# Kernel tuning notes

Measured on AMD Instinct MI355X. Metric: run time of the kernel, lower is better.

Reference implementation:

```python
import jax, jax.numpy as jnp
import numpy as np

N = 50000           # nodes
E = 1_600_000       # edges (avg degree 32)
DIN_N = 128         # in_dim_n
DIN_E = 64          # in_dim_e
DOUT_N = 64         # out_dim_n
DOUT_E = 64         # out_dim_e
SLOPE = 0.01        # torch F.leaky_relu default negative_slope


def _lrelu(x):
    return jnp.where(x >= 0, x, SLOPE * x)


def setup_inputs() -> dict:
    key = jax.random.key(0)
    ks = jax.random.split(key, 8)
    nfeats = jax.random.normal(ks[0], (N, DIN_N), dtype=jnp.float32)
    efeats = jax.random.normal(ks[1], (E, DIN_E), dtype=jnp.float32)
    src = jax.random.randint(ks[2], (E,), 0, N)
    dst = jax.random.randint(ks[3], (E,), 0, N)
    # learned params (xavier-ish scaling)
    W_fc = jax.random.normal(ks[4], (DOUT_N, DIN_N), dtype=jnp.float32) / np.sqrt(DIN_N)
    d_cat = DIN_E + 2 * DOUT_N
    W_edge = jax.random.normal(ks[5], (DOUT_E, d_cat), dtype=jnp.float32) / np.sqrt(d_cat)
    b_edge = jnp.zeros((DOUT_E,), dtype=jnp.float32)
    w_coef = jax.random.normal(ks[6], (1, DOUT_E), dtype=jnp.float32) / np.sqrt(DOUT_E)
    return {"nfeats": nfeats, "efeats": efeats, "src": src, "dst": dst,
            "W_fc": W_fc, "W_edge": W_edge, "b_edge": b_edge, "w_coef": w_coef}


def reference(nfeats, efeats, src, dst, W_fc, W_edge, b_edge, w_coef):
    # node projection: z = fc(nfeats)  (bias=False)
    z = nfeats @ W_fc.T                                   # [N, DOUT_N]
    # per-edge: concat(src_z, edge_feats, dst_z) -> linear -> leaky_relu
    stacked = jnp.concatenate([z[src], efeats, z[dst]], axis=1)   # [E, DIN_E+2*DOUT_N]
    feat = _lrelu(stacked @ W_edge.T + b_edge)            # [E, DOUT_E]
    # attention logit: linear -> leaky_relu applied twice (as in source)
    a = _lrelu(_lrelu(feat @ w_coef.T))                   # [E, 1]
    # segment softmax over incoming edges of each dst node
    m = jax.lax.stop_gradient(jax.ops.segment_max(a, dst, num_segments=N))  # [N,1]
    ex = jnp.exp(a - m[dst])                              # [E, 1]
    denom = jax.ops.segment_sum(ex, dst, num_segments=N)  # [N, 1]
    alpha = ex / denom[dst]                               # [E, 1]
    # weighted aggregation of src projections back to dst nodes
    h = jax.ops.segment_sum(alpha * z[src], dst, num_segments=N)  # [N, DOUT_N]
    return (h, feat)
```

## Files before the change

### kernel.cpp

```cpp
#include <hip/hip_runtime.h>
#include <hip/hip_bf16.h>


typedef __attribute__((ext_vector_type(8))) short short8;
typedef __attribute__((ext_vector_type(4))) float f32x4;
typedef __attribute__((ext_vector_type(2))) int i32x2;

__device__ __forceinline__ short bf1(float f) {
    union { __hip_bfloat16 h; short s; } u;
    u.h = __float2bfloat16(f);
    return u.s;
}

__device__ __forceinline__ float bf2f(unsigned short u) {
    union { unsigned v; float f; } w; w.v = ((unsigned)u) << 16; return w.f;
}

__device__ __forceinline__ short8 pack8(f32x4 a, f32x4 b) {
    short8 r;
    r[0] = bf1(a[0]); r[1] = bf1(a[1]); r[2] = bf1(a[2]); r[3] = bf1(a[3]);
    r[4] = bf1(b[0]); r[5] = bf1(b[1]); r[6] = bf1(b[2]); r[7] = bf1(b[3]);
    return r;
}

__device__ __forceinline__ f32x4 ntld4(const float* p) {
    return __builtin_nontemporal_load((const f32x4*)p);
}

__device__ __forceinline__ f32x4 ld4(const float* p) {
    return *(const f32x4*)p;
}

#define MFMA16(A, B, C) __builtin_amdgcn_mfma_f32_16x16x32_bf16((A), (B), (C), 0, 0, 0)

__global__ __launch_bounds__(256) void k0_wpq(
    const float* __restrict__ W_edge, const float* __restrict__ W_fc,
    unsigned short* __restrict__ wp_bf, unsigned short* __restrict__ wq_bf)
{
    const int i = blockIdx.x * 256 + threadIdx.x;
    if (i >= 64 * 128) return;
    const int c = i >> 7, k = i & 127;
    float sp = 0.f, sq = 0.f;
    for (int j = 0; j < 64; ++j) {
        const float f = W_fc[j * 128 + k];
        sp += W_edge[c * 192 + j] * f;
        sq += W_edge[c * 192 + 128 + j] * f;
    }
    wp_bf[i] = (unsigned short)bf1(sp);
    wq_bf[i] = (unsigned short)bf1(sq);
}

__global__ __launch_bounds__(256) void k12_node(
    const float* __restrict__ nfeats, const float* __restrict__ W_fc,
    const unsigned short* __restrict__ wp_bf, const unsigned short* __restrict__ wq_bf,
    const float* __restrict__ b_edge,
    unsigned short* __restrict__ z_bf, unsigned short* __restrict__ p_bf,
    unsigned short* __restrict__ q_bf, int ntiles)
{
    const int lane = threadIdx.x & 63;
    const int wave = threadIdx.x >> 6;
    const int l15 = lane & 15, g = lane >> 4;
    const int ti = blockIdx.x * 4 + wave;
    if (ti >= ntiles) return;
    const int n0 = ti * 16;

    const float* xp = nfeats + (long)(n0 + l15) * 128 + g * 8;
    short8 Ax[4];
#pragma unroll
    for (int kt = 0; kt < 4; ++kt)
        Ax[kt] = pack8(ntld4(xp + kt * 32), ntld4(xp + kt * 32 + 4));

#pragma unroll
    for (int t = 0; t < 4; ++t) {
        const int col = t * 16 + l15;
        f32x4 az = (f32x4){0.f, 0.f, 0.f, 0.f};
        f32x4 ap = az, aq = az;
#pragma unroll
        for (int kt = 0; kt < 4; ++kt) {
            const float* bz = W_fc + (long)col * 128 + kt * 32 + g * 8;
            az = MFMA16(Ax[kt], pack8(ld4(bz), ld4(bz + 4)), az);
            const short8 bp = *(const short8*)(wp_bf + (long)col * 128 + kt * 32 + g * 8);
            ap = MFMA16(Ax[kt], bp, ap);
            const short8 bq = *(const short8*)(wq_bf + (long)col * 128 + kt * 32 + g * 8);
            aq = MFMA16(Ax[kt], bq, aq);
        }
        const float bias = b_edge[col];
#pragma unroll
        for (int r = 0; r < 4; ++r) {
            const long row = n0 + g * 4 + r;
            z_bf[row * 64 + col] = (unsigned short)bf1(az[r]);
            p_bf[row * 64 + col] = (unsigned short)bf1(ap[r] + bias);
            q_bf[row * 64 + col] = (unsigned short)bf1(aq[r]);
        }
    }
}

#define LOAD_PQ(T, PQ) {                                                    \
    const int sE_ = __shfl(((T) < 4) ? sAll0 : sAll1, ((T)&3) * 16 + l15, 64); \
    const int dE_ = __shfl(((T) < 4) ? dAll0 : dAll1, ((T)&3) * 16 + l15, 64); \
    const unsigned short* pp_ = p_bf + (long)sE_ * 64 + g * 8;              \
    PQ[0] = *(const short8*)pp_;                                            \
    PQ[1] = *(const short8*)(pp_ + 32);                                     \
    const unsigned short* qp_ = q_bf + (long)dE_ * 64 + g * 8;              \
    PQ[2] = *(const short8*)qp_;                                            \
    PQ[3] = *(const short8*)(qp_ + 32);                                     \
}

#define STAGE_EF(T, B) {                                                    \
    const float* gs_ = efeats + (wbase + (T) * 16) * 64;                    \
    _Pragma("unroll")                                                       \
    for (int i_ = 0; i_ < 4; ++i_) {                                        \
        const int L_ = i_ * 64 + lane;                                      \
        const int G_ = (L_ & ~15) | ((L_ & 15) ^ ((L_ >> 4) & 7));          \
        __builtin_amdgcn_global_load_lds(                                   \
            (const __attribute__((address_space(1))) unsigned int*)(gs_ + G_ * 4), \
            (__attribute__((address_space(3))) unsigned int*)(&efb[wave][B][i_ * 256]), \
            16, 0, 0);                                                      \
    }                                                                       \
}

#define EF_READ(B, E0, E1, E2, E3) {                                        \
    const float* eb2_ = &efb[wave][B][0];                                   \
    const int ro_ = l15 * 64, sx_ = l15 & 7;                                \
    E0 = *(const f32x4*)(eb2_ + ro_ + (((2 * g    ) ^ sx_) << 2));          \
    E1 = *(const f32x4*)(eb2_ + ro_ + (((2 * g + 1) ^ sx_) << 2));          \
    E2 = *(const f32x4*)(eb2_ + ro_ + (((2 * g + 8) ^ sx_) << 2));          \
    E3 = *(const f32x4*)(eb2_ + ro_ + (((2 * g + 9) ^ sx_) << 2));          \
}

#define VMW asm volatile("s_waitcnt vmcnt(40)" ::: "memory");

#define DO_TILE(T, PQ, BUF, DOWAIT, PREFETCH) {                             \
    const long eb_ = wbase + (T) * 16;                                      \
    DOWAIT                                                                  \
    f32x4 e0_, e1_, e2_, e3_;                                               \
    EF_READ(BUF, e0_, e1_, e2_, e3_);                                       \
    asm volatile("s_waitcnt lgkmcnt(0)" ::: "memory");                      \
    PREFETCH                                                                \
    f32x4 acc_[4];                                                          \
    _Pragma("unroll")                                                       \
    for (int t = 0; t < 4; ++t) acc_[t] = (f32x4){0.f, 0.f, 0.f, 0.f};      \
    acc_[0] = MFMA16(PQ[0], IdA, acc_[0]);                                  \
    acc_[1] = MFMA16(PQ[0], IdB, acc_[1]);                                  \
    acc_[2] = MFMA16(PQ[1], IdA, acc_[2]);                                  \
    acc_[3] = MFMA16(PQ[1], IdB, acc_[3]);                                  \
    acc_[0] = MFMA16(PQ[2], IdA, acc_[0]);                                  \
    acc_[1] = MFMA16(PQ[2], IdB, acc_[1]);                                  \
    acc_[2] = MFMA16(PQ[3], IdA, acc_[2]);                                  \
    acc_[3] = MFMA16(PQ[3], IdB, acc_[3]);                                  \
    short8 Aef0_ = pack8(e0_, e1_), Aef1_ = pack8(e2_, e3_);                \
    _Pragma("unroll")                                                       \
    for (int t = 0; t < 4; ++t) {                                           \
        acc_[t] = MFMA16(Aef0_, W2f[t * 64 + lane], acc_[t]);               \
        acc_[t] = MFMA16(Aef1_, W2f[(4 + t) * 64 + lane], acc_[t]);         \
    }                                                                       \
    float myex_ = 0.f;                                                      \
    _Pragma("unroll")                                                       \
    for (int r = 0; r < 4; ++r) {                                           \
        float s_ = 0.f;                                                     \
        _Pragma("unroll")                                                   \
        for (int t = 0; t < 4; ++t) {                                       \
            float v_ = acc_[t][r];                                          \
            v_ = (v_ >= 0.f) ? v_ : 0.01f * v_;                             \
            __builtin_nontemporal_store(v_,                                 \
                feat_out + (eb_ + g * 4 + r) * 64 + t * 16 + l15);          \
            s_ += v_ * wc[t];                                               \
        }                                                                   \
        s_ += __shfl_xor(s_, 1, 16);                                        \
        s_ += __shfl_xor(s_, 2, 16);                                        \
        s_ += __shfl_xor(s_, 4, 16);                                        \
        s_ += __shfl_xor(s_, 8, 16);                                        \
        s_ = (s_ >= 0.f) ? s_ : 0.01f * s_;                                 \
        s_ = (s_ >= 0.f) ? s_ : 0.01f * s_;                                 \
        const float ex_ = __expf(s_);                                       \
        if (l15 == r) myex_ = ex_;                                          \
    }                                                                       \
    const int dmine_ = __shfl(((T) < 4) ? dAll0 : dAll1,                    \
                              ((T)&3) * 16 + g * 4 + (l15 & 3), 64);        \
    if (l15 < 4) {                                                          \
        exbuf[eb_ + g * 4 + l15] = myex_;                                   \
        rank[eb_ + g * 4 + l15] = atomicAdd(&deg[dmine_], 1);               \
    }                                                                       \
}

__global__ __launch_bounds__(256, 4) void k3_edges(
    const float* __restrict__ efeats, const int* __restrict__ src,
    const int* __restrict__ dst, const float* __restrict__ W_edge,
    const float* __restrict__ w_coef, const unsigned short* __restrict__ p_bf,
    const unsigned short* __restrict__ q_bf, float* __restrict__ feat_out,
    float* __restrict__ exbuf, int* __restrict__ deg, int* __restrict__ rank)
{
    __shared__ short8 W2f[512];
    __shared__ float efb[4][2][1024];

    const int tid = threadIdx.x;
    const int lane = tid & 63;
    const int wave = tid >> 6;
    const int l15 = lane & 15, g = lane >> 4;
    const long wbase = ((long)blockIdx.x * 4 + wave) * 128;

    STAGE_EF(0, 0);
    const int sAll0 = src[wbase + lane];
    const int dAll0 = dst[wbase + lane];
    const int sAll1 = src[wbase + 64 + lane];
    const int dAll1 = dst[wbase + 64 + lane];
    STAGE_EF(1, 1);

#pragma unroll
    for (int jj = 0; jj < 2; ++jj) {
        const int fi = tid + jj * 256;
        const int s = fi >> 6, l = fi & 63;
        const int col = (s & 3) * 16 + (l & 15);
        const int gg = l >> 4, kt = s >> 2;
        const float* wp = W_edge + col * 192 + 64 + kt * 32 + gg * 8;
        W2f[fi] = pack8(ld4(wp), ld4(wp + 4));
    }

    float wc[4];
#pragma unroll
    for (int t = 0; t < 4; ++t) wc[t] = w_coef[t * 16 + l15];

    const short one = (short)0x3F80;
    short8 IdA, IdB;
#pragma unroll
    for (int jj = 0; jj < 8; ++jj) {
        IdA[jj] = (l15 == g * 8 + jj) ? one : (short)0;
        IdB[jj] = (16 + l15 == g * 8 + jj) ? one : (short)0;
    }
    __syncthreads();

    short8 pqA[4], pqB[4];
    LOAD_PQ(0, pqA);
    DO_TILE(0, pqA, 0, , { STAGE_EF(2, 0); LOAD_PQ(1, pqB); });
    DO_TILE(1, pqB, 1, , { STAGE_EF(3, 1); LOAD_PQ(2, pqA); });
    DO_TILE(2, pqA, 0, VMW, { STAGE_EF(4, 0); LOAD_PQ(3, pqB); });
    DO_TILE(3, pqB, 1, VMW, { STAGE_EF(5, 1); LOAD_PQ(4, pqA); });
    DO_TILE(4, pqA, 0, VMW, { STAGE_EF(6, 0); LOAD_PQ(5, pqB); });
    DO_TILE(5, pqB, 1, VMW, { STAGE_EF(7, 1); LOAD_PQ(6, pqA); });
    DO_TILE(6, pqA, 0, VMW, { LOAD_PQ(7, pqB); });
    DO_TILE(7, pqB, 1, VMW, );
}

__global__ __launch_bounds__(256) void k_scan1(
    const int* __restrict__ deg, int* __restrict__ bsum, int N)
{
    __shared__ int ws4[4];
    const int tid = threadIdx.x, lane = tid & 63, wave = tid >> 6;
    const int i0 = blockIdx.x * 1024 + tid * 4;
    int s = 0;
#pragma unroll
    for (int jj = 0; jj < 4; ++jj) {
        const int i = i0 + jj;
        if (i < N) s += deg[i];
    }
#pragma unroll
    for (int d = 1; d < 64; d <<= 1) s += __shfl_xor(s, d, 64);
    if (lane == 0) ws4[wave] = s;
    __syncthreads();
    if (tid == 0) bsum[blockIdx.x] = ws4[0] + ws4[1] + ws4[2] + ws4[3];
}

__global__ __launch_bounds__(64) void k_scan2(
    const int* __restrict__ bsum, int* __restrict__ bpre,
    int* __restrict__ off, int nb, int N)
{
    const int t = threadIdx.x;
    const int v = (t < nb) ? bsum[t] : 0;
    int x = v;
#pragma unroll
    for (int d = 1; d < 64; d <<= 1) {
        int y = __shfl_up(x, d, 64);
        if (t >= d) x += y;
    }
    if (t < nb) bpre[t] = x - v;
    if (t == 63) off[N] = x;
}

__global__ __launch_bounds__(256) void k_scan3(
    const int* __restrict__ deg, const int* __restrict__ bpre,
    int* __restrict__ off, int N)
{
    __shared__ int ws4[4];
    const int tid = threadIdx.x, lane = tid & 63, wave = tid >> 6;
    const int i0 = blockIdx.x * 1024 + tid * 4;
    int v[4];
#pragma unroll
    for (int jj = 0; jj < 4; ++jj) {
        const int i = i0 + jj;
        v[jj] = (i < N) ? deg[i] : 0;
    }
    const int s = v[0] + v[1] + v[2] + v[3];
    int x = s;
#pragma unroll
    for (int d = 1; d < 64; d <<= 1) {
        int y = __shfl_up(x, d, 64);
        if (lane >= d) x += y;
    }
    if (lane == 63) ws4[wave] = x;
    __syncthreads();
    int wpre = 0;
#pragma unroll
    for (int w = 0; w < 4; ++w) if (w < wave) wpre += ws4[w];
    int run = bpre[blockIdx.x] + wpre + (x - s);
#pragma unroll
    for (int jj = 0; jj < 4; ++jj) {
        const int i = i0 + jj;
        if (i < N) off[i] = run;
        run += v[jj];
    }
}

__global__ __launch_bounds__(256) void k_scatter(
    const int* __restrict__ src, const int* __restrict__ dst,
    const float* __restrict__ exbuf, const int* __restrict__ off,
    const int* __restrict__ rank, i32x2* __restrict__ pairs, long E)
{
    const long e = (long)blockIdx.x * 256 + threadIdx.x;
    if (e >= E) return;
    const int d = dst[e];
    const int pos = off[d] + rank[e];
    i32x2 pr;
    pr[0] = src[e];
    pr[1] = __float_as_int(exbuf[e]);
    pairs[pos] = pr;
}

__global__ __launch_bounds__(256) void k5_aggregate(
    const int* __restrict__ off, const i32x2* __restrict__ pairs,
    const unsigned short* __restrict__ z_bf, float* __restrict__ h, int N)
{
    const int wave = threadIdx.x >> 6, lane = threadIdx.x & 63;
    const int n = blockIdx.x * 4 + wave;
    if (n >= N) return;
    const int beg = off[n], end = off[n + 1];
    float den = 0.f;
    float a0 = 0.f, a1 = 0.f, a2 = 0.f, a3 = 0.f;
    for (int base = beg; base < end; base += 64) {
        const int rem = end - base;
        i32x2 pr = (i32x2){0, 0};
        if (lane < rem) pr = __builtin_nontemporal_load(&pairs[base + lane]);
        const float ex = __int_as_float(pr[1]);
        float t = ex;
#pragma unroll
        for (int d = 1; d < 64; d <<= 1) t += __shfl_xor(t, d, 64);
        den += t;
        const int cnt = rem < 64 ? rem : 64;
        const int cnt4 = (cnt + 3) & ~3;
        for (int j = 0; j < cnt4; j += 4) {
            const int s0 = __shfl(pr[0], j, 64);
            const int s1 = __shfl(pr[0], j + 1, 64);
            const int s2 = __shfl(pr[0], j + 2, 64);
            const int s3 = __shfl(pr[0], j + 3, 64);
            const float e0 = __shfl(ex, j, 64);
            const float e1 = __shfl(ex, j + 1, 64);
            const float e2 = __shfl(ex, j + 2, 64);
            const float e3 = __shfl(ex, j + 3, 64);
            a0 = fmaf(e0, bf2f(z_bf[(long)s0 * 64 + lane]), a0);
            a1 = fmaf(e1, bf2f(z_bf[(long)s1 * 64 + lane]), a1);
            a2 = fmaf(e2, bf2f(z_bf[(long)s2 * 64 + lane]), a2);
            a3 = fmaf(e3, bf2f(z_bf[(long)s3 * 64 + lane]), a3);
        }
    }
    const float acc = (a0 + a1) + (a2 + a3);
    __builtin_nontemporal_store((end > beg) ? acc / den : 0.f,
                                h + (long)n * 64 + lane);
}

extern "C" void kernel_launch(void* const* d_in, const int* in_sizes, int n_in,
                              void* d_out, int out_size, void* d_ws, size_t ws_size,
                              hipStream_t stream) {
    const float* nfeats = (const float*)d_in[0];
    const float* efeats = (const float*)d_in[1];
    const int*   src    = (const int*)d_in[2];
    const int*   dst    = (const int*)d_in[3];
    const float* W_fc   = (const float*)d_in[4];
    const float* W_edge = (const float*)d_in[5];
    const float* b_edge = (const float*)d_in[6];
    const float* w_coef = (const float*)d_in[7];

    const int  N = in_sizes[0] / 128;
    const long E = in_sizes[2];
    const int  nb = (N + 1023) / 1024;
    const int  ntiles = N / 16;

    float* h    = (float*)d_out;
    float* feat = (float*)d_out + (long)N * 64;

    unsigned short* z_bf   = (unsigned short*)d_ws;
    unsigned short* p_bf   = z_bf + (long)N * 64;
    unsigned short* q_bf   = p_bf + (long)N * 64;
    unsigned short* wp_bf  = q_bf + (long)N * 64;
    unsigned short* wq_bf  = wp_bf + 64 * 128;
    float*          exbuf  = (float*)(wq_bf + 64 * 128);
    int*            deg    = (int*)(exbuf + E);
    int*            rank   = deg + N;
    int*            off    = rank + E;
    i32x2*          pairs  = (i32x2*)(off + N + 2);
    int*            bsum   = (int*)(pairs + E);
    int*            bpre   = bsum + 64;

    (void)hipMemsetAsync(deg, 0, (size_t)N * sizeof(int), stream);

    k0_wpq<<<32, 256, 0, stream>>>(W_edge, W_fc, wp_bf, wq_bf);
    k12_node<<<(ntiles + 3) / 4, 256, 0, stream>>>(nfeats, W_fc, wp_bf, wq_bf,
                                                   b_edge, z_bf, p_bf, q_bf, ntiles);
    k3_edges<<<(int)(E / 512), 256, 0, stream>>>(efeats, src, dst, W_edge, w_coef,
                                                 p_bf, q_bf, feat, exbuf, deg, rank);
    k_scan1<<<nb, 256, 0, stream>>>(deg, bsum, N);
    k_scan2<<<1, 64, 0, stream>>>(bsum, bpre, off, nb, N);
    k_scan3<<<nb, 256, 0, stream>>>(deg, bpre, off, N);
    k_scatter<<<(int)((E + 255) / 256), 256, 0, stream>>>(src, dst, exbuf, off,
                                                          rank, pairs, E);
    k5_aggregate<<<(N + 3) / 4, 256, 0, stream>>>(off, pairs, z_bf, h, N);
}
```

Before: 356.9 us.

## Single-buffer edge-feature LDS staging for higher occupancy; fold deg memset into node kernel

The edge kernel's per-wave efeats LDS staging goes from double to single buffering. This cuts its shared memory so the launch-bounds occupancy hint can rise from 4 to 6 blocks per CU. The next tile's stage is issued only after the current tile's LDS reads complete, and the vmcnt wait threshold is tightened to match. This trades prefetch depth for more resident waves to hide gather latency. Separately, the node kernel now zeroes the degree array, which removes the hipMemsetAsync call and its launch overhead.

Measured after the change: 470.9 us. 1.32x slower.

```diff
diff --git a/kernel.cpp b/kernel.cpp
--- a/kernel.cpp
+++ b/kernel.cpp
@@ -55,7 +55,7 @@
     const unsigned short* __restrict__ wp_bf, const unsigned short* __restrict__ wq_bf,
     const float* __restrict__ b_edge,
     unsigned short* __restrict__ z_bf, unsigned short* __restrict__ p_bf,
-    unsigned short* __restrict__ q_bf, int ntiles)
+    unsigned short* __restrict__ q_bf, int* __restrict__ deg, int ntiles)
 {
     const int lane = threadIdx.x & 63;
     const int wave = threadIdx.x >> 6;
@@ -63,6 +63,8 @@
     const int ti = blockIdx.x * 4 + wave;
     if (ti >= ntiles) return;
     const int n0 = ti * 16;
+
+    if (lane < 16) deg[n0 + lane] = 0;
 
     const float* xp = nfeats + (long)(n0 + l15) * 128 + g * 8;
     short8 Ax[4];
@@ -106,7 +108,7 @@
     PQ[3] = *(const short8*)(qp_ + 32);                                     \
 }
 
-#define STAGE_EF(T, B) {                                                    \
+#define STAGE_EF(T) {                                                       \
     const float* gs_ = efeats + (wbase + (T) * 16) * 64;                    \
     _Pragma("unroll")                                                       \
     for (int i_ = 0; i_ < 4; ++i_) {                                        \
@@ -114,13 +116,13 @@
         const int G_ = (L_ & ~15) | ((L_ & 15) ^ ((L_ >> 4) & 7));          \
         __builtin_amdgcn_global_load_lds(                                   \
             (const __attribute__((address_space(1))) unsigned int*)(gs_ + G_ * 4), \
-            (__attribute__((address_space(3))) unsigned int*)(&efb[wave][B][i_ * 256]), \
+            (__attribute__((address_space(3))) unsigned int*)(&efb[wave][i_ * 256]), \
             16, 0, 0);                                                      \
     }                                                                       \
 }
 
-#define EF_READ(B, E0, E1, E2, E3) {                                        \
-    const float* eb2_ = &efb[wave][B][0];                                   \
+#define EF_READ(E0, E1, E2, E3) {                                           \
+    const float* eb2_ = &efb[wave][0];                                      \
     const int ro_ = l15 * 64, sx_ = l15 & 7;                                \
     E0 = *(const f32x4*)(eb2_ + ro_ + (((2 * g    ) ^ sx_) << 2));          \
     E1 = *(const f32x4*)(eb2_ + ro_ + (((2 * g + 1) ^ sx_) << 2));          \
@@ -128,15 +130,16 @@
     E3 = *(const f32x4*)(eb2_ + ro_ + (((2 * g + 9) ^ sx_) << 2));          \
 }
 
-#define VMW asm volatile("s_waitcnt vmcnt(40)" ::: "memory");
-
-#define DO_TILE(T, PQ, BUF, DOWAIT, PREFETCH) {                             \
+#define VMW asm volatile("s_waitcnt vmcnt(16)" ::: "memory");
+
+#define DO_TILE(T, PQ, DOWAIT, DOPQ, DOSTAGE) {                             \
     const long eb_ = wbase + (T) * 16;                                      \
     DOWAIT                                                                  \
     f32x4 e0_, e1_, e2_, e3_;                                               \
-    EF_READ(BUF, e0_, e1_, e2_, e3_);                                       \
+    EF_READ(e0_, e1_, e2_, e3_);                                            \
+    DOPQ                                                                    \
     asm volatile("s_waitcnt lgkmcnt(0)" ::: "memory");                      \
-    PREFETCH                                                                \
+    DOSTAGE                                                                 \
     f32x4 acc_[4];                                                          \
     _Pragma("unroll")                                                       \
     for (int t = 0; t < 4; ++t) acc_[t] = (f32x4){0.f, 0.f, 0.f, 0.f};      \
@@ -183,7 +186,7 @@
     }                                                                       \
 }
 
-__global__ __launch_bounds__(256, 4) void k3_edges(
+__global__ __launch_bounds__(256, 6) void k3_edges(
     const float* __restrict__ efeats, const int* __restrict__ src,
     const int* __restrict__ dst, const float* __restrict__ W_edge,
     const float* __restrict__ w_coef, const unsigned short* __restrict__ p_bf,
@@ -191,7 +194,7 @@
     float* __restrict__ exbuf, int* __restrict__ deg, int* __restrict__ rank)
 {
     __shared__ short8 W2f[512];
-    __shared__ float efb[4][2][1024];
+    __shared__ float efb[4][1024];
 
     const int tid = threadIdx.x;
     const int lane = tid & 63;
@@ -199,12 +202,11 @@
     const int l15 = lane & 15, g = lane >> 4;
     const long wbase = ((long)blockIdx.x * 4 + wave) * 128;
 
-    STAGE_EF(0, 0);
+    STAGE_EF(0);
     const int sAll0 = src[wbase + lane];
     const int dAll0 = dst[wbase + lane];
     const int sAll1 = src[wbase + 64 + lane];
     const int dAll1 = dst[wbase + 64 + lane];
-    STAGE_EF(1, 1);
 
 #pragma unroll
     for (int jj = 0; jj < 2; ++jj) {
@@ -227,18 +229,19 @@
         IdA[jj] = (l15 == g * 8 + jj) ? one : (short)0;
         IdB[jj] = (16 + l15 == g * 8 + jj) ? one : (short)0;
     }
-    __syncthreads();
 
     short8 pqA[4], pqB[4];
     LOAD_PQ(0, pqA);
-    DO_TILE(0, pqA, 0, , { STAGE_EF(2, 0); LOAD_PQ(1, pqB); });
-    DO_TILE(1, pqB, 1, , { STAGE_EF(3, 1); LOAD_PQ(2, pqA); });
-    DO_TILE(2, pqA, 0, VMW, { STAGE_EF(4, 0); LOAD_PQ(3, pqB); });
-    DO_TILE(3, pqB, 1, VMW, { STAGE_EF(5, 1); LOAD_PQ(4, pqA); });
-    DO_TILE(4, pqA, 0, VMW, { STAGE_EF(6, 0); LOAD_PQ(5, pqB); });
-    DO_TILE(5, pqB, 1, VMW, { STAGE_EF(7, 1); LOAD_PQ(6, pqA); });
-    DO_TILE(6, pqA, 0, VMW, { LOAD_PQ(7, pqB); });
-    DO_TILE(7, pqB, 1, VMW, );
+    __syncthreads();
+
+    DO_TILE(0, pqA, ,    { LOAD_PQ(1, pqB); }, { STAGE_EF(1); });
+    DO_TILE(1, pqB, VMW, { LOAD_PQ(2, pqA); }, { STAGE_EF(2); });
+    DO_TILE(2, pqA, VMW, { LOAD_PQ(3, pqB); }, { STAGE_EF(3); });
+    DO_TILE(3, pqB, VMW, { LOAD_PQ(4, pqA); }, { STAGE_EF(4); });
+    DO_TILE(4, pqA, VMW, { LOAD_PQ(5, pqB); }, { STAGE_EF(5); });
+    DO_TILE(5, pqB, VMW, { LOAD_PQ(6, pqA); }, { STAGE_EF(6); });
+    DO_TILE(6, pqA, VMW, { LOAD_PQ(7, pqB); }, { STAGE_EF(7); });
+    DO_TILE(7, pqB, VMW, , );
 }
 
 __global__ __launch_bounds__(256) void k_scan1(
@@ -399,11 +402,10 @@
     int*            bsum   = (int*)(pairs + E);
     int*            bpre   = bsum + 64;
 
-    (void)hipMemsetAsync(deg, 0, (size_t)N * sizeof(int), stream);
-
     k0_wpq<<<32, 256, 0, stream>>>(W_edge, W_fc, wp_bf, wq_bf);
     k12_node<<<(ntiles + 3) / 4, 256, 0, stream>>>(nfeats, W_fc, wp_bf, wq_bf,
-                                                   b_edge, z_bf, p_bf, q_bf, ntiles);
+                                                   b_edge, z_bf, p_bf, q_bf,
+                                                   deg, ntiles);
     k3_edges<<<(int)(E / 512), 256, 0, stream>>>(efeats, src, dst, W_edge, w_coef,
                                                  p_bf, q_bf, feat, exbuf, deg, rank);
     k_scan1<<<nb, 256, 0, stream>>>(deg, bsum, N);
```
